# Optimization experiments

Measured on AMD Instinct MI355X. Metric: run time of the kernel, lower is better.

Reference implementation:

```python
import jax, jax.numpy as jnp
import numpy as np

B, N, F_IN, F_OUT = 4, 4096, 64, 64
ALPHA = 0.2   # leakyrelu negative slope
M_MIX = 0.8   # self.m
NEG_INF = -1e12


def setup_inputs() -> dict:
    key = jax.random.key(0)
    k1, k2, k3, k4 = jax.random.split(key, 4)
    inp = jax.random.normal(k1, (B, N, F_IN), dtype=jnp.float32)
    adj = jax.random.uniform(k2, (B, N, N), dtype=jnp.float32)
    # xavier_uniform with gain=1.414
    limW = 1.414 * np.sqrt(6.0 / (F_IN + F_OUT))
    W = jax.random.uniform(k3, (F_IN, F_OUT), dtype=jnp.float32, minval=-limW, maxval=limW)
    lima = 1.414 * np.sqrt(6.0 / (2 * F_OUT + 1))
    a = jax.random.uniform(k4, (2 * F_OUT, 1), dtype=jnp.float32, minval=-lima, maxval=lima)
    return {"inp": inp, "adj": adj, "W": W, "a": a}


def reference(inp, adj, W, a):
    # h: [B, N, F_OUT]
    h = jnp.einsum("bnf,fo->bno", inp, W)
    # The torch code builds a_input[b,i,j] = [h_i ; h_j], applies leakyrelu
    # elementwise, then contracts with a. Since leakyrelu is elementwise,
    # e[b,i,j] = lrelu(h_i) @ a[:F] + lrelu(h_j) @ a[F:], exactly.
    lh = jax.nn.leaky_relu(h, negative_slope=ALPHA)          # [B, N, F_OUT]
    f_src = lh @ a[:F_OUT, 0]                                # [B, N]  (h_i term)
    f_dst = lh @ a[F_OUT:, 0]                                # [B, N]  (h_j term)
    e = f_src[:, :, None] + f_dst[:, None, :]                # [B, N, N]
    dj = M_MIX * adj + (1.0 - M_MIX) * e
    attention = jnp.where(dj > 0, dj, NEG_INF)
    # torch softmax over dim=1 (the i axis)
    attention = jax.nn.softmax(attention, axis=1)
    # dropout is identity in eval mode
    h_prime = jnp.einsum("bij,bjo->bio", attention, h)       # [B, N, F_OUT]
    return jax.nn.relu(h_prime)
```

## Files before the change

### kernel.cpp

```cpp
#include <hip/hip_runtime.h>
#include <hip/hip_bf16.h>


#define Bn 4
#define Nn 4096
#define KS 8
#define IC 64

typedef _Float16 half8 __attribute__((ext_vector_type(8)));
typedef _Float16 half4 __attribute__((ext_vector_type(4)));
typedef float f32x4 __attribute__((ext_vector_type(4)));
typedef float f4v __attribute__((ext_vector_type(4)));

__global__ __launch_bounds__(256) void k_prep(
    const float* __restrict__ inp, const float* __restrict__ W,
    const float* __restrict__ a, float* __restrict__ h,
    float* __restrict__ fsrc, float* __restrict__ fdst) {
  __shared__ float Ws[64 * 64];
  __shared__ float as[128];
  __shared__ float xs[4][64];
  const int t = threadIdx.x;
  for (int k = t; k < 4096; k += 256) Ws[k] = W[k];
  if (t < 128) as[t] = a[t];
  const int w = t >> 6;
  const int o = t & 63;
  const int row = blockIdx.x * 4 + w;
  xs[w][o] = inp[(size_t)row * 64 + o];
  __syncthreads();
  float acc = 0.f;
  const float* xr = xs[w];
#pragma unroll
  for (int f = 0; f < 64; ++f) acc += xr[f] * Ws[f * 64 + o];
  h[(size_t)row * 64 + o] = acc;
  float lh = acc > 0.f ? acc : 0.2f * acc;
  float vs = lh * as[o];
  float vd = lh * as[64 + o];
#pragma unroll
  for (int off = 32; off > 0; off >>= 1) {
    vs += __shfl_down(vs, off);
    vd += __shfl_down(vd, off);
  }
  if (o == 0) { fsrc[row] = vs; fdst[row] = vd; }
}

__global__ __launch_bounds__(256) void k_estats(
    const float* __restrict__ adj, const float* __restrict__ fsrc,
    const float* __restrict__ fdst, _Float16* __restrict__ E,
    float* __restrict__ pm) {
  const int t = threadIdx.x;
  const int jb = blockIdx.x, ic = blockIdx.y, b = blockIdx.z;
  const int j = jb * 1024 + t * 4;
  const int i0 = ic * 64;
  __shared__ float fss[64];
  if (t < 64) fss[t] = fsrc[b * Nn + i0 + t];
  __syncthreads();
  const float4 fd = *(const float4*)&fdst[b * Nn + j];
  const f4v* ap = (const f4v*)(adj + ((size_t)(b * Nn + i0)) * Nn + j);
  _Float16* ep = E + ((size_t)(b * Nn + i0)) * Nn + j;
  float s0 = 0.f, s1 = 0.f, s2 = 0.f, s3 = 0.f;
#pragma unroll 4
  for (int ii = 0; ii < 64; ++ii) {
    f4v v = __builtin_nontemporal_load(ap + (size_t)ii * 1024);
    float fi = fss[ii];
    float d0 = 0.8f * v.x + 0.2f * (fi + fd.x);
    float d1 = 0.8f * v.y + 0.2f * (fi + fd.y);
    float d2 = 0.8f * v.z + 0.2f * (fi + fd.z);
    float d3 = 0.8f * v.w + 0.2f * (fi + fd.w);
    float e0 = d0 > 0.f ? __expf(d0) : 0.f;
    float e1 = d1 > 0.f ? __expf(d1) : 0.f;
    float e2 = d2 > 0.f ? __expf(d2) : 0.f;
    float e3 = d3 > 0.f ? __expf(d3) : 0.f;
    s0 += e0; s1 += e1; s2 += e2; s3 += e3;
    half4 e;
    e[0] = (_Float16)e0; e[1] = (_Float16)e1;
    e[2] = (_Float16)e2; e[3] = (_Float16)e3;
    *(half4*)(ep + (size_t)ii * Nn) = e;
  }
  float4 sv; sv.x = s0; sv.y = s1; sv.z = s2; sv.w = s3;
  *(float4*)&pm[((size_t)(ic * Bn + b)) * Nn + j] = sv;
}

__global__ __launch_bounds__(256) void k_hscale(
    const float* __restrict__ h, const float* __restrict__ pm,
    _Float16* __restrict__ hT) {
  const int t = threadIdx.x;
  const int jt = blockIdx.x, b = blockIdx.y;
  __shared__ _Float16 hl[64][72];
  __shared__ float sis[64];
  if (t < 64) {
    const int j = jt * 64 + t;
    float sv = 0.f;
#pragma unroll 8
    for (int ic = 0; ic < IC; ++ic) sv += pm[((size_t)(ic * Bn + b)) * Nn + j];
    sis[t] = sv > 0.f ? 1.0f / sv : 0.f;
  }
  __syncthreads();
#pragma unroll
  for (int r = 0; r < 4; ++r) {
    const int jl = r * 16 + (t >> 4);
    const int j = jt * 64 + jl;
    const int o4 = (t & 15) * 4;
    float si = sis[jl];
    float4 hv = *(const float4*)&h[((size_t)(b * Nn + j)) * 64 + o4];
    hl[o4 + 0][jl] = (_Float16)(hv.x * si);
    hl[o4 + 1][jl] = (_Float16)(hv.y * si);
    hl[o4 + 2][jl] = (_Float16)(hv.z * si);
    hl[o4 + 3][jl] = (_Float16)(hv.w * si);
  }
  __syncthreads();
#pragma unroll
  for (int r = 0; r < 2; ++r) {
    const int o = r * 32 + (t >> 3);
    const int ch = t & 7;
    half8 v = *(half8*)&hl[o][ch * 8];
    *(half8*)&hT[((size_t)(b * 64 + o)) * 4096 + jt * 64 + ch * 8] = v;
  }
}

__global__ __launch_bounds__(256) void k_attnmm(
    const _Float16* __restrict__ E, const _Float16* __restrict__ hT,
    float* __restrict__ part) {
  const int t = threadIdx.x;
  const int ks = blockIdx.x;
  const int ib = blockIdx.y;
  const int b = blockIdx.z;
  const int i0 = ib * 64;
  const int kbase = ks * 512;
  const int w = t >> 6;
  const int lane = t & 63;

  __shared__ _Float16 hs[64][136];

  f32x4 acc[4];
#pragma unroll
  for (int nt = 0; nt < 4; ++nt)
#pragma unroll
    for (int r = 0; r < 4; ++r) acc[nt][r] = 0.f;

  const int ai = i0 + w * 16 + (lane & 15);
  const int ko = (lane >> 4) * 8;
  const half8* Erow = (const half8*)(E + ((size_t)(b * Nn + ai)) * Nn + kbase + ko);
  const int so = t >> 2;
  const int sk = (t & 3) * 32;
  const _Float16* hTrow = hT + ((size_t)(b * 64 + so)) * Nn + kbase + sk;

  for (int ch = 0; ch < 4; ++ch) {
    const int k0 = ch * 128;
    __syncthreads();
#pragma unroll
    for (int q = 0; q < 4; ++q) {
      half8 v = *(const half8*)(hTrow + k0 + q * 8);
      *(half8*)&hs[so][sk + q * 8] = v;
    }
    __syncthreads();
#pragma unroll
    for (int kt = 0; kt < 4; ++kt) {
      half8 af = __builtin_nontemporal_load((const half8*)((const _Float16*)Erow + k0 + kt * 32));
#pragma unroll
      for (int nt = 0; nt < 4; ++nt) {
        half8 bf = *(const half8*)&hs[nt * 16 + (lane & 15)][kt * 32 + ko];
        acc[nt] = __builtin_amdgcn_mfma_f32_16x16x32_f16(af, bf, acc[nt], 0, 0, 0);
      }
    }
  }
#pragma unroll
  for (int nt = 0; nt < 4; ++nt)
#pragma unroll
    for (int r = 0; r < 4; ++r) {
      const int i = i0 + w * 16 + (lane >> 4) * 4 + r;
      const int o = nt * 16 + (lane & 15);
      part[(((size_t)ks * Bn + b) * Nn + i) * 64 + o] = acc[nt][r];
    }
}

__global__ __launch_bounds__(256) void k_final(
    const float* __restrict__ part, float* __restrict__ out) {
  const int e = blockIdx.x * 256 + threadIdx.x;
  const f4v* p4 = (const f4v*)part;
  f4v sv = __builtin_nontemporal_load(p4 + e);
  const size_t stride = (size_t)Bn * Nn * 64 / 4;
#pragma unroll
  for (int ks = 1; ks < KS; ++ks) {
    f4v v = __builtin_nontemporal_load(p4 + (size_t)ks * stride + e);
    sv.x += v.x; sv.y += v.y; sv.z += v.z; sv.w += v.w;
  }
  float4 r;
  r.x = fmaxf(sv.x, 0.f); r.y = fmaxf(sv.y, 0.f);
  r.z = fmaxf(sv.z, 0.f); r.w = fmaxf(sv.w, 0.f);
  ((float4*)out)[e] = r;
}

extern "C" void kernel_launch(void* const* d_in, const int* in_sizes, int n_in,
                              void* d_out, int out_size, void* d_ws, size_t ws_size,
                              hipStream_t stream) {
  const float* inp = (const float*)d_in[0];
  const float* adj = (const float*)d_in[1];
  const float* W   = (const float*)d_in[2];
  const float* a   = (const float*)d_in[3];
  float* out = (float*)d_out;

  float* ws   = (float*)d_ws;
  float* h    = ws;
  float* fsrc = h + 1048576;
  float* fdst = fsrc + 16384;
  float* pm   = fdst + 16384;
  float* part = pm + (size_t)IC * Bn * Nn;
  _Float16* hT = (_Float16*)(part + (size_t)KS * Bn * Nn * 64);
  _Float16* E  = hT + (size_t)Bn * 64 * Nn;

  k_prep<<<Bn * Nn / 4, 256, 0, stream>>>(inp, W, a, h, fsrc, fdst);
  k_estats<<<dim3(4, IC, Bn), 256, 0, stream>>>(adj, fsrc, fdst, E, pm);
  k_hscale<<<dim3(64, Bn), 256, 0, stream>>>(h, pm, hT);
  k_attnmm<<<dim3(KS, 64, Bn), 256, 0, stream>>>(E, hT, part);
  k_final<<<Bn * Nn * 64 / 4 / 256, 256, 0, stream>>>(part, out);
}
```

Before: 438.3 us.

## Drop LDS staging in attention matmul, widen row tile, halve K-split

The attention-times-h matmul no longer stages hT through shared memory with barriers. Each wave now loads B fragments directly from global/L2 and computes a 32x64 tile with two A fragments. The K-split drops from 8 to 4, which halves the partial-sum buffer and the reduction traffic in the final kernel. In exchange, each wave re-reads hT from cache without LDS sharing, and the grid has a quarter as many blocks.

New measurement: 449.7 us. 2.6% more time.

```diff
diff --git a/kernel.cpp b/kernel.cpp
--- a/kernel.cpp
+++ b/kernel.cpp
@@ -4,7 +4,7 @@
 
 #define Bn 4
 #define Nn 4096
-#define KS 8
+#define KS 4
 #define IC 64
 
 typedef _Float16 half8 __attribute__((ext_vector_type(8)));
@@ -124,53 +124,52 @@
   const int ks = blockIdx.x;
   const int ib = blockIdx.y;
   const int b = blockIdx.z;
-  const int i0 = ib * 64;
-  const int kbase = ks * 512;
   const int w = t >> 6;
   const int lane = t & 63;
 
-  __shared__ _Float16 hs[64][136];
-
-  f32x4 acc[4];
-#pragma unroll
-  for (int nt = 0; nt < 4; ++nt)
-#pragma unroll
-    for (int r = 0; r < 4; ++r) acc[nt][r] = 0.f;
-
-  const int ai = i0 + w * 16 + (lane & 15);
-  const int ko = (lane >> 4) * 8;
-  const half8* Erow = (const half8*)(E + ((size_t)(b * Nn + ai)) * Nn + kbase + ko);
-  const int so = t >> 2;
-  const int sk = (t & 3) * 32;
-  const _Float16* hTrow = hT + ((size_t)(b * 64 + so)) * Nn + kbase + sk;
-
-  for (int ch = 0; ch < 4; ++ch) {
-    const int k0 = ch * 128;
-    __syncthreads();
-#pragma unroll
-    for (int q = 0; q < 4; ++q) {
-      half8 v = *(const half8*)(hTrow + k0 + q * 8);
-      *(half8*)&hs[so][sk + q * 8] = v;
-    }
-    __syncthreads();
-#pragma unroll
-    for (int kt = 0; kt < 4; ++kt) {
-      half8 af = __builtin_nontemporal_load((const half8*)((const _Float16*)Erow + k0 + kt * 32));
-#pragma unroll
-      for (int nt = 0; nt < 4; ++nt) {
-        half8 bf = *(const half8*)&hs[nt * 16 + (lane & 15)][kt * 32 + ko];
-        acc[nt] = __builtin_amdgcn_mfma_f32_16x16x32_f16(af, bf, acc[nt], 0, 0, 0);
+  const int i0 = ib * 128 + w * 32;
+  const int kbase = ks * (Nn / KS);
+  const int rlane = lane & 15;
+  const int klane = (lane >> 4) * 8;
+
+  f32x4 acc[2][4];
+#pragma unroll
+  for (int m = 0; m < 2; ++m)
+#pragma unroll
+    for (int n = 0; n < 4; ++n)
+#pragma unroll
+      for (int r = 0; r < 4; ++r) acc[m][n][r] = 0.f;
+
+  const _Float16* Ep0 = E + ((size_t)(b * Nn + i0 + rlane)) * Nn + kbase + klane;
+  const _Float16* Ep1 = Ep0 + (size_t)16 * Nn;
+  const _Float16* hp  = hT + ((size_t)(b * 64 + rlane)) * Nn + kbase + klane;
+
+#pragma unroll 4
+  for (int k = 0; k < Nn / KS; k += 32) {
+    half8 af[2], bf[4];
+    af[0] = __builtin_nontemporal_load((const half8*)(Ep0 + k));
+    af[1] = __builtin_nontemporal_load((const half8*)(Ep1 + k));
+#pragma unroll
+    for (int n = 0; n < 4; ++n)
+      bf[n] = *(const half8*)(hp + (size_t)(n * 16) * Nn + k);
+#pragma unroll
+    for (int m = 0; m < 2; ++m)
+#pragma unroll
+      for (int n = 0; n < 4; ++n)
+        acc[m][n] = __builtin_amdgcn_mfma_f32_16x16x32_f16(af[m], bf[n], acc[m][n], 0, 0, 0);
+  }
+
+  const int r0 = (lane >> 4) * 4;
+#pragma unroll
+  for (int m = 0; m < 2; ++m)
+#pragma unroll
+    for (int n = 0; n < 4; ++n)
+#pragma unroll
+      for (int r = 0; r < 4; ++r) {
+        const int i = i0 + m * 16 + r0 + r;
+        const int o = n * 16 + rlane;
+        part[(((size_t)ks * Bn + b) * Nn + i) * 64 + o] = acc[m][n][r];
       }
-    }
-  }
-#pragma unroll
-  for (int nt = 0; nt < 4; ++nt)
-#pragma unroll
-    for (int r = 0; r < 4; ++r) {
-      const int i = i0 + w * 16 + (lane >> 4) * 4 + r;
-      const int o = nt * 16 + (lane & 15);
-      part[(((size_t)ks * Bn + b) * Nn + i) * 64 + o] = acc[nt][r];
-    }
 }
 
 __global__ __launch_bounds__(256) void k_final(
@@ -211,6 +210,6 @@
   k_prep<<<Bn * Nn / 4, 256, 0, stream>>>(inp, W, a, h, fsrc, fdst);
   k_estats<<<dim3(4, IC, Bn), 256, 0, stream>>>(adj, fsrc, fdst, E, pm);
   k_hscale<<<dim3(64, Bn), 256, 0, stream>>>(h, pm, hT);
-  k_attnmm<<<dim3(KS, 64, Bn), 256, 0, stream>>>(E, hT, part);
+  k_attnmm<<<dim3(KS, 32, Bn), 256, 0, stream>>>(E, hT, part);
   k_final<<<Bn * Nn * 64 / 4 / 256, 256, 0, stream>>>(part, out);
 }
```
